# Kernel tuning notes

Hardware: AMD Instinct MI355X
Metric: run time of the kernel (lower is better)

## Reference

```python
import jax, jax.numpy as jnp
import numpy as np

OUT, IN, V, K, R = 4096, 4096, 8, 4096, 128
TOKENS = 8192

def setup_inputs() -> dict:
    key = jax.random.key(0)
    ks = jax.random.split(key, 9)
    return {
        "x": jax.random.normal(ks[0], (TOKENS, IN), dtype=jnp.float32),
        "centroids": jax.random.normal(ks[1], (K, V), dtype=jnp.float32),
        "indices": jax.random.randint(ks[2], (OUT, IN // V), 0, K, dtype=jnp.int32),
        "U": jax.random.normal(ks[3], (OUT, R), dtype=jnp.float32) * 0.02,
        "S": jax.random.uniform(ks[4], (R,), dtype=jnp.float32) + 0.1,
        "Vt": jax.random.normal(ks[5], (R, IN), dtype=jnp.float32) * 0.02,
        "weight_scale": jax.random.uniform(ks[6], (OUT,), dtype=jnp.float32) + 0.5,
        "weight_bias": jax.random.normal(ks[7], (OUT,), dtype=jnp.float32) * 0.01,
        "bias": jax.random.normal(ks[8], (OUT,), dtype=jnp.float32),
    }

def dequant_weight(centroids, indices, U, S, Vt, weight_scale, weight_bias):
    # codebook lookup: [OUT, IN//V] indices -> [OUT, IN//V, V] -> [OUT, IN]
    w_q = centroids[indices].reshape(indices.shape[0], -1)
    # per-output-channel affine
    w_q = w_q * weight_scale[:, None] + weight_bias[:, None]
    # low-rank SVD correction: U @ diag(S) @ Vt
    lowrank = jnp.einsum('or,r,ri->oi', U, S, Vt)
    return w_q + lowrank

def reference(x, centroids, indices, U, S, Vt, weight_scale, weight_bias, bias):
    dtype = x.dtype
    weight = dequant_weight(centroids, indices, U, S, Vt, weight_scale, weight_bias)
    # result = x @ W^T + bias  (as in forward)
    result = x @ weight.T.astype(dtype) + bias.astype(dtype)[None, :]
    return result.astype(dtype)
```

## Files before the change

### kernel.cpp

```cpp
#include <hip/hip_runtime.h>
#include <hip/hip_bf16.h>
#include <stdint.h>

using bf16 = __hip_bfloat16;
typedef __bf16 bf16x8 __attribute__((ext_vector_type(8)));
typedef float f32x4 __attribute__((ext_vector_type(4)));
typedef short short8 __attribute__((ext_vector_type(8)));

#define GLD_LDS16(gp, lp)                                                            \
  __builtin_amdgcn_global_load_lds(                                                  \
      (const __attribute__((address_space(1))) unsigned int*)(gp),                   \
      (__attribute__((address_space(3))) unsigned int*)(lp), 16, 0, 0)

__global__ __launch_bounds__(256) void convert_x_kernel(const float* __restrict__ x,
                                                        bf16* __restrict__ xb, int n)
{
  for (int i = (blockIdx.x * 256 + threadIdx.x) * 8; i < n; i += gridDim.x * 256 * 8) {
    float4 a = *(const float4*)(x + i);
    float4 b = *(const float4*)(x + i + 4);
    union { bf16 h[8]; short8 v; } u;
    u.h[0] = __float2bfloat16(a.x);
    u.h[1] = __float2bfloat16(a.y);
    u.h[2] = __float2bfloat16(a.z);
    u.h[3] = __float2bfloat16(a.w);
    u.h[4] = __float2bfloat16(b.x);
    u.h[5] = __float2bfloat16(b.y);
    u.h[6] = __float2bfloat16(b.z);
    u.h[7] = __float2bfloat16(b.w);
    *(short8*)(xb + i) = u.v;
  }
}

__global__ __launch_bounds__(256) void prep_kernel(const float* __restrict__ U,
                                                   const float* __restrict__ S,
                                                   const float* __restrict__ Vt,
                                                   bf16* __restrict__ Ub,
                                                   bf16* __restrict__ SVtT)
{
  int t = blockIdx.x * 256 + threadIdx.x;
  if (t < 4096 * 128) {
    Ub[t] = __float2bfloat16(U[t]);
    int i = t >> 7, r = t & 127;
    SVtT[t] = __float2bfloat16(S[r] * Vt[r * 4096 + i]);
  }
}

__global__ __launch_bounds__(256, 2) void gemm_wbuild(const bf16* __restrict__ A,
                                                      const bf16* __restrict__ B,
                                                      bf16* __restrict__ Cb,
                                                      int M, int N, int K,
                                                      const int* __restrict__ indices,
                                                      const float* __restrict__ centroids,
                                                      const float* __restrict__ wscale,
                                                      const float* __restrict__ wbias)
{
  __shared__ bf16 As4[4 * 4096];
  __shared__ bf16 Bs4[4 * 4096];

  const int tid  = threadIdx.x;
  const int m0   = blockIdx.y * 128;
  const int n0   = blockIdx.x * 128;
  const int wid  = tid >> 6;
  const int lane = tid & 63;
  const int wm   = wid >> 1;
  const int wn   = wid & 1;
  const int kk   = (lane >> 4) * 8;
  const int fr   = lane & 15;

  const int sr = tid >> 2;
  const int sc = (tid & 3) * 8;
  const bf16* ga = A + (size_t)(m0 + sr) * 128 + sc;
  const bf16* gb = B + (size_t)(n0 + sr) * 128 + sc;

#pragma unroll
  for (int c = 0; c < 4; c++) {
    GLD_LDS16(ga + 32 * c,            &As4[c * 4096 + tid * 8]);
    GLD_LDS16(ga + 32 * c + 64 * 128, &As4[c * 4096 + 2048 + tid * 8]);
    GLD_LDS16(gb + 32 * c,            &Bs4[c * 4096 + tid * 8]);
    GLD_LDS16(gb + 32 * c + 64 * 128, &Bs4[c * 4096 + 2048 + tid * 8]);
  }
  __syncthreads();

  f32x4 acc[4][4] = {};
#pragma unroll
  for (int c = 0; c < 4; c++) {
    bf16x8 af[4], bfr[4];
#pragma unroll
    for (int m = 0; m < 4; m++)
      af[m] = *(const bf16x8*)(&As4[c * 4096 + (wm * 64 + m * 16 + fr) * 32 + kk]);
#pragma unroll
    for (int n = 0; n < 4; n++)
      bfr[n] = *(const bf16x8*)(&Bs4[c * 4096 + (wn * 64 + n * 16 + fr) * 32 + kk]);
#pragma unroll
    for (int m = 0; m < 4; m++)
#pragma unroll
      for (int n = 0; n < 4; n++)
        acc[m][n] = __builtin_amdgcn_mfma_f32_16x16x32_bf16(af[m], bfr[n], acc[m][n], 0, 0, 0);
  }

#pragma unroll
  for (int m = 0; m < 4; m++) {
#pragma unroll
    for (int n = 0; n < 4; n++) {
      const int col  = n0 + wn * 64 + n * 16 + (lane & 15);
      const int rowb = m0 + wm * 64 + m * 16 + (lane >> 4) * 4;
#pragma unroll
      for (int j = 0; j < 4; j++) {
        const int row  = rowb + j;
        const int idxv = indices[row * 512 + (col >> 3)];
        const float cv = centroids[idxv * 8 + (col & 7)];
        const float w  = cv * wscale[row] + wbias[row] + acc[m][n][j];
        Cb[(size_t)row * N + col] = __float2bfloat16(w);
      }
    }
  }
}

__global__ __launch_bounds__(512, 2) void gemm256(const bf16* __restrict__ A,
                                                  const bf16* __restrict__ B,
                                                  float* __restrict__ C,
                                                  const float* __restrict__ bias)
{
  extern __shared__ char smem[];
  constexpr int K = 4096;
  constexpr int N = 4096;

  const int tid  = threadIdx.x;
  const int lane = tid & 63;
  const int wave = tid >> 6;
  const int wm   = wave >> 2;
  const int wn   = wave & 3;
  const int fr   = lane & 15;
  const int kk   = (lane >> 4) * 8;
  const int swx  = (fr & 7) << 4;

  const int bid = blockIdx.x;
  const int xcd = bid & 7;
  const int idx = bid >> 3;
  const int mi  = (xcd & 3) * 8 + (idx & 7);
  const int ni  = (xcd >> 2) * 8 + (idx >> 3);
  const int m0  = mi * 256;
  const int n0  = ni * 256;

  const int pA = tid * 16;
  const int rA = pA >> 7;
  const int kA = ((pA ^ ((rA & 7) << 4)) & 127) >> 1;
  const bf16* gA0 = A + (size_t)(m0 + rA) * K + kA;
  const int pB = (tid >> 8) * 8192 + (tid & 255) * 16;
  const int rB = pB >> 7;
  const int kB = ((pB ^ ((rB & 7) << 4)) & 127) >> 1;
  const bf16* gB0 = B + (size_t)(n0 + rB) * K + kB;

  f32x4 acc[8][4] = {};

  const int laneK0 = fr * 128 + ((kk * 2) ^ swx);
  const int laneK1 = fr * 128 + ((64 + kk * 2) ^ swx);
  const char* bA00 = smem + wm * 16384 + laneK0;
  const char* bA01 = smem + wm * 16384 + laneK1;
  const char* bA10 = bA00 + 65536;
  const char* bA11 = bA01 + 65536;
  const char* bB00 = smem + 32768 + wn * 8192 + laneK0;
  const char* bB01 = smem + 32768 + wn * 8192 + laneK1;
  const char* bB10 = bB00 + 65536;
  const char* bB11 = bB01 + 65536;

#define STG_A0(bo) GLD_LDS16(gA_p,                   smem + (bo) + pA)
#define STG_A1(bo) GLD_LDS16(gA_p + 128 * 4096,      smem + (bo) + pA + 16384)
#define STG_A2(bo) GLD_LDS16(gA_p +  64 * 4096,      smem + (bo) + pA + 8192)
#define STG_A3(bo) GLD_LDS16(gA_p + 192 * 4096,      smem + (bo) + pA + 24576)
#define STG_B0(bo) GLD_LDS16(gB_p,                   smem + (bo) + 32768 + pB)
#define STG_B1(bo) GLD_LDS16(gB_p + 128 * 4096,      smem + (bo) + 32768 + pB + 16384)
#define STG_B2(bo) GLD_LDS16(gB_p + 64 +  32 * 4096, smem + (bo) + 32768 + pB + 4096)
#define STG_B3(bo) GLD_LDS16(gB_p + 64 + 160 * 4096, smem + (bo) + 32768 + pB + 20480)

#define LOAD_AQ(dst, qm, P0, P1)                                                    \
  _Pragma("unroll") for (int mm = 0; mm < 4; mm++)                                  \
    _Pragma("unroll") for (int ks = 0; ks < 2; ks++)                                \
      dst[mm][ks] = *(const bf16x8*)((ks ? (P1) : (P0)) +                           \
                                     ((qm) * 8192 + mm * 2048));

#define LOAD_BQ(dst, qn, P0, P1)                                                    \
  _Pragma("unroll") for (int nn = 0; nn < 2; nn++)                                  \
    _Pragma("unroll") for (int ks = 0; ks < 2; ks++)                                \
      dst[nn][ks] = *(const bf16x8*)((ks ? (P1) : (P0)) +                           \
                                     ((qn) * 4096 + nn * 2048));

#define CLUSTER(qm, qn, av, bv)                                                     \
  __builtin_amdgcn_s_setprio(1);                                                    \
  _Pragma("unroll") for (int ks = 0; ks < 2; ks++)                                  \
    _Pragma("unroll") for (int mm = 0; mm < 4; mm++)                                \
      _Pragma("unroll") for (int nn = 0; nn < 2; nn++)                              \
        acc[(qm) * 4 + mm][(qn) * 2 + nn] =                                         \
            __builtin_amdgcn_mfma_f32_16x16x32_bf16(                                \
                av[mm][ks], bv[nn][ks], acc[(qm) * 4 + mm][(qn) * 2 + nn],          \
                0, 0, 0);                                                           \
  __builtin_amdgcn_s_setprio(0);

#define SBAR   __builtin_amdgcn_s_barrier()
#define SCHED0 __builtin_amdgcn_sched_barrier(0)
#define VM4    asm volatile("s_waitcnt vmcnt(4)" ::: "memory")

  bf16x8 aq0[4][2], aq1[4][2], b0[2][2], b1[2][2], b0r[2][2];

  GLD_LDS16(gA0,                  smem + pA);
  GLD_LDS16(gA0 + 128 * 4096,     smem + pA + 16384);
  GLD_LDS16(gB0,                  smem + 32768 + pB);
  GLD_LDS16(gB0 + 128 * 4096,     smem + 32768 + pB + 16384);
  GLD_LDS16(gB0 +  32 * 4096,     smem + 32768 + pB + 4096);
  GLD_LDS16(gB0 + 160 * 4096,     smem + 32768 + pB + 20480);
  GLD_LDS16(gA0 +  64 * 4096,     smem + pA + 8192);
  GLD_LDS16(gA0 + 192 * 4096,     smem + pA + 24576);
  GLD_LDS16(gA0 + 64,             smem + 65536 + pA);
  GLD_LDS16(gA0 + 64 + 128 * 4096, smem + 65536 + pA + 16384);
  GLD_LDS16(gB0 + 64 +  32 * 4096, smem + 65536 + 32768 + pB + 4096);
  GLD_LDS16(gB0 + 64 + 160 * 4096, smem + 65536 + 32768 + pB + 20480);
  GLD_LDS16(gA0 + 64 +  64 * 4096, smem + 65536 + pA + 8192);
  GLD_LDS16(gA0 + 64 + 192 * 4096, smem + 65536 + pA + 24576);
  asm volatile("s_waitcnt vmcnt(6)" ::: "memory");
  SBAR;
  LOAD_AQ(aq0, 0, bA00, bA01);
  LOAD_BQ(b0, 0, bB00, bB01);
  SCHED0;

  const bf16* gA_p = gA0 + 128;
  const bf16* gB_p = gB0 + 64;

#define TILE(AB, NB, ABa0, ABa1, ABb0, ABb1, NBa0, NBa1, NBb0, NBb1)                \
  {                                                                                 \
                    \
    SBAR;                                                                           \
    STG_B0(NB); STG_B1(NB);                                                         \
    LOAD_BQ(b1, 1, ABb0, ABb1);                                                     \
    SCHED0;                                                                         \
    CLUSTER(0, 0, aq0, b0);                                                         \
    SCHED0;                                                                         \
                  \
    SBAR;                                                                           \
    STG_A0(AB); STG_A1(AB);                                                         \
    SCHED0;                                                                         \
    CLUSTER(0, 1, aq0, b1);                                                         \
    SCHED0;                                                                         \
    LOAD_AQ(aq1, 1, ABa0, ABa1);                                                    \
    SCHED0;                                                                         \
                   \
    SBAR;                                                                           \
    STG_B2(AB); STG_B3(AB);                                                         \
    LOAD_BQ(b0r, 0, ABb0, ABb1);                                                    \
    SCHED0;                                                                         \
    CLUSTER(1, 1, aq1, b1);                                                         \
    SCHED0;                                                                         \
    \
    VM4;                                                                            \
    SBAR;                                                                           \
    STG_A2(AB); STG_A3(AB);                                                         \
    SCHED0;                                                                         \
    CLUSTER(1, 0, aq1, b0r);                                                        \
    SCHED0;                                                                         \
    LOAD_AQ(aq0, 0, NBa0, NBa1);                                                    \
    LOAD_BQ(b0, 0, NBb0, NBb1);                                                     \
    SCHED0;                                                                         \
    gA_p += 64; gB_p += 64;                                                         \
  }

  for (int tt = 0; tt < 32; tt++) {
    TILE(0, 65536, bA00, bA01, bB00, bB01, bA10, bA11, bB10, bB11);
    TILE(65536, 0, bA10, bA11, bB10, bB11, bA00, bA01, bB00, bB01);
  }

#pragma unroll
  for (int mf = 0; mf < 8; mf++) {
#pragma unroll
    for (int nf = 0; nf < 4; nf++) {
      const int col  = n0 + wn * 64 + nf * 16 + fr;
      const int row0 = m0 + wm * 128 + mf * 16 + (lane >> 4) * 4;
      const float bv = bias[col];
#pragma unroll
      for (int j = 0; j < 4; j++)
        C[(size_t)(row0 + j) * N + col] = acc[mf][nf][j] + bv;
    }
  }
#undef TILE
#undef CLUSTER
#undef LOAD_AQ
#undef LOAD_BQ
#undef SBAR
#undef SCHED0
#undef VM4
#undef STG_A0
#undef STG_A1
#undef STG_A2
#undef STG_A3
#undef STG_B0
#undef STG_B1
#undef STG_B2
#undef STG_B3
}

extern "C" void kernel_launch(void* const* d_in, const int* in_sizes, int n_in,
                              void* d_out, int out_size, void* d_ws, size_t ws_size,
                              hipStream_t stream)
{
  const float* x         = (const float*)d_in[0];
  const float* centroids = (const float*)d_in[1];
  const int*   indices   = (const int*)d_in[2];
  const float* U         = (const float*)d_in[3];
  const float* S         = (const float*)d_in[4];
  const float* Vt        = (const float*)d_in[5];
  const float* wscale    = (const float*)d_in[6];
  const float* wbias     = (const float*)d_in[7];
  const float* bias      = (const float*)d_in[8];
  float* out = (float*)d_out;

  char* ws = (char*)d_ws;
  bf16* xb   = (bf16*)(ws);
  bf16* Wb   = (bf16*)(ws + 67108864);
  bf16* Ub   = (bf16*)(ws + 100663296);
  bf16* SVtT = (bf16*)(ws + 101711872);

  convert_x_kernel<<<2048, 256, 0, stream>>>(x, xb, 8192 * 4096);
  prep_kernel<<<2048, 256, 0, stream>>>(U, S, Vt, Ub, SVtT);

  dim3 gW(4096 / 128, 4096 / 128);
  gemm_wbuild<<<gW, 256, 0, stream>>>(Ub, SVtT, Wb, 4096, 4096, 128,
                                      indices, centroids, wscale, wbias);

  gemm256<<<512, 512, 131072, stream>>>(xb, Wb, out, bias);
}
```

Before: 288.3 us.

## Fuse x conversion, low-rank prep and weight build into one launch

Merges the three pre-GEMM kernels into a single launch. Blocks 0-1023 build the dequantized weight tile: they read U and S*Vt directly as fp32, convert them to bf16 in registers and stage them through shared memory, so the Ub/SVtT intermediates are gone. The remaining 2048 blocks convert x to bf16 at the same time. This removes two launches and the round trip through the intermediate buffers, and lets the weight-build work overlap with the bandwidth-bound x conversion. The cost is a scalar transposed shared-memory store for the Vt tile, which may cause bank conflicts, and extra syncs in each K step.

```diff
diff --git a/kernel.cpp b/kernel.cpp
--- a/kernel.cpp
+++ b/kernel.cpp
@@ -12,106 +12,123 @@
       (const __attribute__((address_space(1))) unsigned int*)(gp),                   \
       (__attribute__((address_space(3))) unsigned int*)(lp), 16, 0, 0)
 
-__global__ __launch_bounds__(256) void convert_x_kernel(const float* __restrict__ x,
-                                                        bf16* __restrict__ xb, int n)
+__global__ __launch_bounds__(256) void fused_pre(const float* __restrict__ x,
+                                                 bf16* __restrict__ xb, int n,
+                                                 const float* __restrict__ U,
+                                                 const float* __restrict__ S,
+                                                 const float* __restrict__ Vt,
+                                                 const int* __restrict__ indices,
+                                                 const float* __restrict__ centroids,
+                                                 const float* __restrict__ wscale,
+                                                 const float* __restrict__ wbias,
+                                                 bf16* __restrict__ Wb)
 {
-  for (int i = (blockIdx.x * 256 + threadIdx.x) * 8; i < n; i += gridDim.x * 256 * 8) {
-    float4 a = *(const float4*)(x + i);
-    float4 b = *(const float4*)(x + i + 4);
-    union { bf16 h[8]; short8 v; } u;
-    u.h[0] = __float2bfloat16(a.x);
-    u.h[1] = __float2bfloat16(a.y);
-    u.h[2] = __float2bfloat16(a.z);
-    u.h[3] = __float2bfloat16(a.w);
-    u.h[4] = __float2bfloat16(b.x);
-    u.h[5] = __float2bfloat16(b.y);
-    u.h[6] = __float2bfloat16(b.z);
-    u.h[7] = __float2bfloat16(b.w);
-    *(short8*)(xb + i) = u.v;
-  }
-}
-
-__global__ __launch_bounds__(256) void prep_kernel(const float* __restrict__ U,
-                                                   const float* __restrict__ S,
-                                                   const float* __restrict__ Vt,
-                                                   bf16* __restrict__ Ub,
-                                                   bf16* __restrict__ SVtT)
-{
-  int t = blockIdx.x * 256 + threadIdx.x;
-  if (t < 4096 * 128) {
-    Ub[t] = __float2bfloat16(U[t]);
-    int i = t >> 7, r = t & 127;
-    SVtT[t] = __float2bfloat16(S[r] * Vt[r * 4096 + i]);
-  }
-}
-
-__global__ __launch_bounds__(256, 2) void gemm_wbuild(const bf16* __restrict__ A,
-                                                      const bf16* __restrict__ B,
-                                                      bf16* __restrict__ Cb,
-                                                      int M, int N, int K,
-                                                      const int* __restrict__ indices,
-                                                      const float* __restrict__ centroids,
-                                                      const float* __restrict__ wscale,
-                                                      const float* __restrict__ wbias)
-{
-  __shared__ bf16 As4[4 * 4096];
-  __shared__ bf16 Bs4[4 * 4096];
-
-  const int tid  = threadIdx.x;
-  const int m0   = blockIdx.y * 128;
-  const int n0   = blockIdx.x * 128;
-  const int wid  = tid >> 6;
-  const int lane = tid & 63;
-  const int wm   = wid >> 1;
-  const int wn   = wid & 1;
-  const int kk   = (lane >> 4) * 8;
-  const int fr   = lane & 15;
-
-  const int sr = tid >> 2;
-  const int sc = (tid & 3) * 8;
-  const bf16* ga = A + (size_t)(m0 + sr) * 128 + sc;
-  const bf16* gb = B + (size_t)(n0 + sr) * 128 + sc;
-
-#pragma unroll
-  for (int c = 0; c < 4; c++) {
-    GLD_LDS16(ga + 32 * c,            &As4[c * 4096 + tid * 8]);
-    GLD_LDS16(ga + 32 * c + 64 * 128, &As4[c * 4096 + 2048 + tid * 8]);
-    GLD_LDS16(gb + 32 * c,            &Bs4[c * 4096 + tid * 8]);
-    GLD_LDS16(gb + 32 * c + 64 * 128, &Bs4[c * 4096 + 2048 + tid * 8]);
-  }
-  __syncthreads();
-
-  f32x4 acc[4][4] = {};
-#pragma unroll
-  for (int c = 0; c < 4; c++) {
-    bf16x8 af[4], bfr[4];
-#pragma unroll
-    for (int m = 0; m < 4; m++)
-      af[m] = *(const bf16x8*)(&As4[c * 4096 + (wm * 64 + m * 16 + fr) * 32 + kk]);
-#pragma unroll
-    for (int n = 0; n < 4; n++)
-      bfr[n] = *(const bf16x8*)(&Bs4[c * 4096 + (wn * 64 + n * 16 + fr) * 32 + kk]);
-#pragma unroll
-    for (int m = 0; m < 4; m++)
-#pragma unroll
-      for (int n = 0; n < 4; n++)
-        acc[m][n] = __builtin_amdgcn_mfma_f32_16x16x32_bf16(af[m], bfr[n], acc[m][n], 0, 0, 0);
-  }
-
-#pragma unroll
-  for (int m = 0; m < 4; m++) {
-#pragma unroll
-    for (int n = 0; n < 4; n++) {
-      const int col  = n0 + wn * 64 + n * 16 + (lane & 15);
-      const int rowb = m0 + wm * 64 + m * 16 + (lane >> 4) * 4;
-#pragma unroll
-      for (int j = 0; j < 4; j++) {
-        const int row  = rowb + j;
-        const int idxv = indices[row * 512 + (col >> 3)];
-        const float cv = centroids[idxv * 8 + (col & 7)];
-        const float w  = cv * wscale[row] + wbias[row] + acc[m][n][j];
-        Cb[(size_t)row * N + col] = __float2bfloat16(w);
+  __shared__ bf16 As[128 * 32];
+  __shared__ bf16 Bs[128 * 32];
+  const int b = blockIdx.x;
+  const int t = threadIdx.x;
+
+  if (b < 1024) {
+    const int m0   = (b >> 5) * 128;
+    const int n0   = (b & 31) * 128;
+    const int wid  = t >> 6;
+    const int lane = t & 63;
+    const int wm   = wid >> 1;
+    const int wn   = wid & 1;
+    const int kk   = (lane >> 4) * 8;
+    const int fr   = lane & 15;
+
+    const int arow = t >> 1;
+    const int ak0  = (t & 1) * 16;
+    const int br   = t >> 3;
+    const int bi0  = (t & 7) * 16;
+
+    f32x4 acc[4][4] = {};
+
+#pragma unroll
+    for (int c = 0; c < 4; c++) {
+      const float* ua = U + (size_t)(m0 + arow) * 128 + c * 32 + ak0;
+      float4 a0 = *(const float4*)(ua);
+      float4 a1 = *(const float4*)(ua + 4);
+      float4 a2 = *(const float4*)(ua + 8);
+      float4 a3 = *(const float4*)(ua + 12);
+      union { bf16 h[8]; short8 v; } pa, pb;
+      pa.h[0] = __float2bfloat16(a0.x); pa.h[1] = __float2bfloat16(a0.y);
+      pa.h[2] = __float2bfloat16(a0.z); pa.h[3] = __float2bfloat16(a0.w);
+      pa.h[4] = __float2bfloat16(a1.x); pa.h[5] = __float2bfloat16(a1.y);
+      pa.h[6] = __float2bfloat16(a1.z); pa.h[7] = __float2bfloat16(a1.w);
+      pb.h[0] = __float2bfloat16(a2.x); pb.h[1] = __float2bfloat16(a2.y);
+      pb.h[2] = __float2bfloat16(a2.z); pb.h[3] = __float2bfloat16(a2.w);
+      pb.h[4] = __float2bfloat16(a3.x); pb.h[5] = __float2bfloat16(a3.y);
+      pb.h[6] = __float2bfloat16(a3.z); pb.h[7] = __float2bfloat16(a3.w);
+
+      const float s = S[c * 32 + br];
+      const float* va = Vt + (size_t)(c * 32 + br) * 4096 + n0 + bi0;
+      float4 v0 = *(const float4*)(va);
+      float4 v1 = *(const float4*)(va + 4);
+      float4 v2 = *(const float4*)(va + 8);
+      float4 v3 = *(const float4*)(va + 12);
+      bf16 bh[16];
+      bh[0]  = __float2bfloat16(s * v0.x); bh[1]  = __float2bfloat16(s * v0.y);
+      bh[2]  = __float2bfloat16(s * v0.z); bh[3]  = __float2bfloat16(s * v0.w);
+      bh[4]  = __float2bfloat16(s * v1.x); bh[5]  = __float2bfloat16(s * v1.y);
+      bh[6]  = __float2bfloat16(s * v1.z); bh[7]  = __float2bfloat16(s * v1.w);
+      bh[8]  = __float2bfloat16(s * v2.x); bh[9]  = __float2bfloat16(s * v2.y);
+      bh[10] = __float2bfloat16(s * v2.z); bh[11] = __float2bfloat16(s * v2.w);
+      bh[12] = __float2bfloat16(s * v3.x); bh[13] = __float2bfloat16(s * v3.y);
+      bh[14] = __float2bfloat16(s * v3.z); bh[15] = __float2bfloat16(s * v3.w);
+
+      __syncthreads();
+
+      *(short8*)(&As[arow * 32 + ak0])     = pa.v;
+      *(short8*)(&As[arow * 32 + ak0 + 8]) = pb.v;
+#pragma unroll
+      for (int j = 0; j < 16; j++)
+        Bs[(bi0 + j) * 32 + br] = bh[j];
+
+      __syncthreads();
+
+      bf16x8 af[4], bfr[4];
+#pragma unroll
+      for (int m = 0; m < 4; m++)
+        af[m] = *(const bf16x8*)(&As[(wm * 64 + m * 16 + fr) * 32 + kk]);
+#pragma unroll
+      for (int nn = 0; nn < 4; nn++)
+        bfr[nn] = *(const bf16x8*)(&Bs[(wn * 64 + nn * 16 + fr) * 32 + kk]);
+#pragma unroll
+      for (int m = 0; m < 4; m++)
+#pragma unroll
+        for (int nn = 0; nn < 4; nn++)
+          acc[m][nn] = __builtin_amdgcn_mfma_f32_16x16x32_bf16(af[m], bfr[nn], acc[m][nn], 0, 0, 0);
+    }
+
+#pragma unroll
+    for (int m = 0; m < 4; m++) {
+#pragma unroll
+      for (int nn = 0; nn < 4; nn++) {
+        const int col  = n0 + wn * 64 + nn * 16 + (lane & 15);
+        const int rowb = m0 + wm * 64 + m * 16 + (lane >> 4) * 4;
+#pragma unroll
+        for (int j = 0; j < 4; j++) {
+          const int row  = rowb + j;
+          const int idxv = indices[row * 512 + (col >> 3)];
+          const float cv = centroids[idxv * 8 + (col & 7)];
+          const float w  = cv * wscale[row] + wbias[row] + acc[m][nn][j];
+          Wb[(size_t)row * 4096 + col] = __float2bfloat16(w);
+        }
       }
+    }
+  } else {
+    const int vb = b - 1024;
+    for (int i = (vb * 256 + t) * 8; i < n; i += 2048 * 256 * 8) {
+      float4 a = *(const float4*)(x + i);
+      float4 c = *(const float4*)(x + i + 4);
+      union { bf16 h[8]; short8 v; } u;
+      u.h[0] = __float2bfloat16(a.x); u.h[1] = __float2bfloat16(a.y);
+      u.h[2] = __float2bfloat16(a.z); u.h[3] = __float2bfloat16(a.w);
+      u.h[4] = __float2bfloat16(c.x); u.h[5] = __float2bfloat16(c.y);
+      u.h[6] = __float2bfloat16(c.z); u.h[7] = __float2bfloat16(c.w);
+      *(short8*)(xb + i) = u.v;
     }
   }
 }
@@ -312,17 +329,11 @@
   float* out = (float*)d_out;
 
   char* ws = (char*)d_ws;
-  bf16* xb   = (bf16*)(ws);
-  bf16* Wb   = (bf16*)(ws + 67108864);
-  bf16* Ub   = (bf16*)(ws + 100663296);
-  bf16* SVtT = (bf16*)(ws + 101711872);
-
-  convert_x_kernel<<<2048, 256, 0, stream>>>(x, xb, 8192 * 4096);
-  prep_kernel<<<2048, 256, 0, stream>>>(U, S, Vt, Ub, SVtT);
-
-  dim3 gW(4096 / 128, 4096 / 128);
-  gemm_wbuild<<<gW, 256, 0, stream>>>(Ub, SVtT, Wb, 4096, 4096, 128,
-                                      indices, centroids, wscale, wbias);
+  bf16* xb = (bf16*)(ws);
+  bf16* Wb = (bf16*)(ws + 67108864);
+
+  fused_pre<<<3072, 256, 0, stream>>>(x, xb, 8192 * 4096, U, S, Vt,
+                                      indices, centroids, wscale, wbias, Wb);
 
   gemm256<<<512, 512, 131072, stream>>>(xb, Wb, out, bias);
 }
```

After: 282.6 us. 2.0% less time.
